# Optimization experiments

Measured on AMD Instinct MI355X. Metric: run time of the kernel, lower is better.

The kernel has to match this reference:

```python
import jax, jax.numpy as jnp
import numpy as np


def setup_inputs() -> dict:
    key = jax.random.key(0)
    k1, k2 = jax.random.split(key)
    B, C, H, W = 4, 256, 64, 64
    hw = 1024  # hs = ws = 32, rate = H/hs = 2
    ori_x = jax.random.normal(k1, (B, C, H, W), dtype=jnp.float32)
    scores = jax.random.uniform(k2, (B, hw, hw), dtype=jnp.float32)
    alpha = jnp.ones((1,), dtype=jnp.float32)
    return {"ori_x": ori_x, "scores": scores, "alpha": alpha}


def reference(ori_x, scores, alpha):
    # GroupConvAttention forward for H=W=64 (no bilinear resize branch taken,
    # matching the torch code's else-branch), rate even (no extra rep-pad).
    B, C, H, W = ori_x.shape
    hw = scores.shape[2]
    hs = int(np.sqrt(hw)); ws = hs
    rate = H // hs               # 2
    vk = 2 * rate                # vksize = 4
    pad = rate // 2              # vpadding = 1 (rate even)

    # extract_patches: ReplicationPad2d(pad) + unfold(kernel=vk, stride=rate)
    x_pad = jnp.pad(ori_x, ((0, 0), (0, 0), (pad, pad), (pad, pad)), mode="edge")
    # gather index grids: patch (m,n), intra-patch (u,v)
    ri = (jnp.arange(hs) * rate)[:, None] + jnp.arange(vk)[None, :]  # [hs, vk]
    ci = (jnp.arange(ws) * rate)[:, None] + jnp.arange(vk)[None, :]  # [ws, vk]
    R = ri[:, None, :, None]   # [hs,1,vk,1]
    Cc = ci[None, :, None, :]  # [1,ws,1,vk]
    value = x_pad[:, :, R, Cc]  # [B, C, hs, ws, vk, vk]

    # conv_transpose2d(scores_, value, stride=rate, padding=pad, groups=B)
    # == per query grid cell (Q,R): combined patch = sum_p scores[b,q,p]*value[b,p]
    s = scores.reshape(B, hs, ws, hs, ws)  # [b, Qy, Qx, my, mx]
    P = jnp.einsum("bQRmn,bcmnuv->bcQRuv", s, value)  # [B,C,hs,ws,vk,vk]

    # overlap-add patches at stride `rate` into padded canvas, then crop padding
    canvas = jnp.zeros((B, C, (hs - 1) * rate + vk, (ws - 1) * rate + vk), P.dtype)
    canvas = canvas.at[:, :, R, Cc].add(P)
    y = canvas[:, :, pad:pad + H, pad:pad + W] / 4.0

    return ori_x + y * alpha
```

## Files before the change

### kernel.cpp

```cpp
#include <hip/hip_runtime.h>
#include <hip/hip_bf16.h>
#include <hip/hip_fp16.h>

#define BB 4
#define CC 256
#define HH 64
#define WW 64
#define QRN 1024
#define KN  1024
#define KDIM 1152
#define TROWS 1089

typedef _Float16 f16x8 __attribute__((ext_vector_type(8)));
typedef float f32x4 __attribute__((ext_vector_type(4)));

#define TP_ELEMS ((size_t)BB * TROWS * KDIM)
#define BP_ELEMS ((size_t)16 * CC * KDIM)


__device__ __forceinline__
void process_qr(const float* __restrict__ sb, _Float16* __restrict__ T,
                int b, int qr, int t) {
    const int Qa = (qr * 993) >> 15;
    const int Ra = qr - 33 * Qa;
    const bool q0 = (Qa < 32), q1 = (Qa >= 1);
    const bool r0 = (Ra < 32), r1 = (Ra >= 1);
    const float* rb00 = sb + ((size_t)((Qa)     * 32 + (Ra)))     * KN;
    const float* rb01 = sb + ((size_t)((Qa)     * 32 + (Ra - 1))) * KN;
    const float* rb10 = sb + ((size_t)((Qa - 1) * 32 + (Ra)))     * KN;
    const float* rb11 = sb + ((size_t)((Qa - 1) * 32 + (Ra - 1))) * KN;
    _Float16* trow = T + ((size_t)b * TROWS + qr) * KDIM;

    float v[5];
    #pragma unroll
    for (int j = 0; j < 5; ++j) {
        const int k = j * 256 + t;
        v[j] = 0.f;
        if (k < KDIM) {
            const int mp = (k * 993) >> 15;
            const int np = k - 33 * mp;
            const bool m0 = (mp < 32), m1 = (mp >= 1) && (mp < 33);
            const bool n0 = (np < 32), n1 = (np >= 1);
            const int col = (mp << 5) + np;
            if (q0 & r0 & m0 & n0) v[j] += rb00[col];
            if (q0 & r1 & m0 & n1) v[j] += rb01[col - 1];
            if (q1 & r0 & m1 & n0) v[j] += rb10[col - 32];
            if (q1 & r1 & m1 & n1) v[j] += rb11[col - 33];
        }
    }
    #pragma unroll
    for (int j = 0; j < 5; ++j) {
        const int k = j * 256 + t;
        if (k < KDIM) trow[k] = (_Float16)v[j];
    }
}

#define T_BLOCKS 545
#define PER_B    705
#define TB_NWG   (BB * PER_B)

__global__ __launch_bounds__(256)
void build_TB(const float* __restrict__ s, const float* __restrict__ x,
              _Float16* __restrict__ T, _Float16* __restrict__ Bp) {
    const int orig = blockIdx.x;
    const int xcd = orig & 7, pos = orig >> 3;
    const int q = TB_NWG / 8, r = TB_NWG % 8;
    const int wgid =
        (xcd < r ? xcd * (q + 1) : r * (q + 1) + (xcd - r) * q) + pos;

    const int b = wgid / PER_B;
    const int rem = wgid - b * PER_B;
    const int t = threadIdx.x;

    if (rem < T_BLOCKS) {
        const float* sb = s + (size_t)b * QRN * KN;
        const int qr0 = rem * 2;
        process_qr(sb, T, b, qr0, t);
        if (qr0 + 1 < TROWS) process_qr(sb, T, b, qr0 + 1, t);
    } else {
        const int u = rem - T_BLOCKS;
        const int rest = u / 5;
        const int kc = u - rest * 5;
        const int cls = rest >> 3, cg = rest & 7;
        const int k = kc * 256 + t;
        if (k >= KDIM) return;
        const int ph = cls >> 1, pw = cls & 1;
        const int ua = 1 - ph, va = 1 - pw;
        const int bc = b * 4 + cls;

        const int mp = (k * 993) >> 15;
        const int np = k - 33 * mp;
        int rr = 2 * mp + ua - 1; rr = min(max(rr, 0), HH - 1);
        int cc2 = 2 * np + va - 1; cc2 = min(max(cc2, 0), WW - 1);
        const int off = rr * WW + cc2;

        const float* xb = x + ((size_t)b * CC + cg * 32) * HH * WW;
        _Float16* bpb = Bp + ((size_t)bc * CC + cg * 32) * KDIM + k;

        #pragma unroll 8
        for (int i = 0; i < 32; ++i) {
            bpb[(size_t)i * KDIM] = (_Float16)xb[(size_t)i * HH * WW + off];
        }
    }
}

__device__ __forceinline__ void gload16(const _Float16* g, _Float16* l) {
    __builtin_amdgcn_global_load_lds(
        (const __attribute__((address_space(1))) unsigned int*)g,
        (__attribute__((address_space(3))) unsigned int*)l, 16, 0, 0);
}

#define NSTEP  36
#define BUF_H  8192
__global__ __launch_bounds__(256, 1)
void gemm_f16(const _Float16* __restrict__ T,
              const _Float16* __restrict__ Bp,
              const float* __restrict__ orix,
              const float* __restrict__ alphap,
              float* __restrict__ out) {
    __shared__ __align__(16) _Float16 smem_h[8 * BUF_H];

    const int lin = blockIdx.x + 2 * (blockIdx.y + 8 * blockIdx.z);
    const int wid = (lin & 7) * 32 + (lin >> 3);
    const int bc  = wid >> 4;
    const int byy = (wid >> 1) & 7;
    const int bxx = wid & 1;

    const int b = bc >> 2, cls = bc & 3;
    const int ph = cls >> 1, pw = cls & 1;
    const int c0  = bxx * 128;
    const int px0 = byy * 128;

    const int t = threadIdx.x;
    const int wv = t >> 6, l = t & 63;
    const int lr = l & 15;
    const int lk = l >> 4;
    const int wr = wv >> 1, wc = wv & 1;

    const _Float16* Ag = Bp + ((size_t)bc * CC + c0) * KDIM;
    const _Float16* Tg = T + (size_t)b * TROWS * KDIM;

    const int st_row = t >> 2, st_slot = t & 3;
    const _Float16* srcA0 = Ag + (size_t)st_row * KDIM + st_slot * 8;
    const _Float16* srcA1 = Ag + (size_t)(st_row + 64) * KDIM + st_slot * 8;
    const int pxr0 = px0 + st_row, pxr1 = px0 + st_row + 64;
    const int trow0 = ((pxr0 >> 5) + ph) * 33 + (pxr0 & 31) + pw;
    const int trow1 = ((pxr1 >> 5) + ph) * 33 + (pxr1 & 31) + pw;
    const _Float16* srcB0 = Tg + (size_t)trow0 * KDIM + st_slot * 8;
    const _Float16* srcB1 = Tg + (size_t)trow1 * KDIM + st_slot * 8;
    _Float16* dst0 = smem_h + t * 8;
    _Float16* dst1 = smem_h + 2048 + t * 8;

    #define ISSUE(ts2)                                                     \
        do {                                                               \
            const int _bo = ((ts2) & 7) * BUF_H;                           \
            const int _k0 = (ts2) * 32;                                    \
            gload16(srcA0 + _k0, dst0 + _bo);                              \
            gload16(srcA1 + _k0, dst1 + _bo);                              \
            gload16(srcB0 + _k0, dst0 + _bo + 4096);                       \
            gload16(srcB1 + _k0, dst1 + _bo + 4096);                       \
        } while (0)

    f32x4 acc[4][4];
    #pragma unroll
    for (int i = 0; i < 4; ++i)
        #pragma unroll
        for (int j = 0; j < 4; ++j)
            acc[i][j] = (f32x4){0.f, 0.f, 0.f, 0.f};

    ISSUE(0); ISSUE(1); ISSUE(2); ISSUE(3); ISSUE(4); ISSUE(5); ISSUE(6);

    #pragma unroll
    for (int ts = 0; ts < NSTEP; ++ts) {
        asm volatile("s_waitcnt vmcnt(24)" ::: "memory");
        __builtin_amdgcn_s_barrier();
        const int nxt = (ts + 7 < NSTEP) ? ts + 7 : NSTEP - 1;
        ISSUE(nxt);

        const _Float16* ab = smem_h + (ts & 7) * BUF_H;
        const _Float16* bb = ab + 4096;
        f16x8 af[4], bf[4];
        #pragma unroll
        for (int mt = 0; mt < 4; ++mt)
            af[mt] = *(const f16x8*)(ab + (wr * 64 + mt * 16 + lr) * 32 + lk * 8);
        #pragma unroll
        for (int nt2 = 0; nt2 < 4; ++nt2)
            bf[nt2] = *(const f16x8*)(bb + (wc * 64 + nt2 * 16 + lr) * 32 + lk * 8);
        __builtin_amdgcn_s_setprio(1);
        #pragma unroll
        for (int mt = 0; mt < 4; ++mt)
            #pragma unroll
            for (int nt2 = 0; nt2 < 4; ++nt2)
                acc[mt][nt2] = __builtin_amdgcn_mfma_f32_16x16x32_f16(
                    af[mt], bf[nt2], acc[mt][nt2], 0, 0, 0);
        __builtin_amdgcn_s_setprio(0);
    }
    #undef ISSUE
    asm volatile("s_waitcnt vmcnt(0)" ::: "memory");

    const float scale = 0.25f * alphap[0];
    #pragma unroll
    for (int mt = 0; mt < 4; ++mt) {
        #pragma unroll
        for (int nt2 = 0; nt2 < 4; ++nt2) {
            #pragma unroll
            for (int r2 = 0; r2 < 4; ++r2) {
                int c  = c0 + wr * 64 + mt * 16 + lk * 4 + r2;
                int px = px0 + wc * 64 + nt2 * 16 + lr;
                int hh = px >> 5, ww2 = px & 31;
                int h = 2 * hh + ph, wp = 2 * ww2 + pw;
                size_t idx = (((size_t)b * CC + c) * HH + h) * WW + wp;
                out[idx] = orix[idx] + scale * acc[mt][nt2][r2];
            }
        }
    }
}

#define TILE_M 64
#define TILE_N 64
#define TILE_K 16

__global__ void copy_kernel(const float* __restrict__ src,
                            float* __restrict__ dst, int n4) {
    int i = blockIdx.x * blockDim.x + threadIdx.x;
    if (i < n4)
        reinterpret_cast<float4*>(dst)[i] =
            reinterpret_cast<const float4*>(src)[i];
}

__global__ void transpose_kernel(const float* __restrict__ x,
                                 float* __restrict__ xT) {
    __shared__ float tile[32][33];
    int bh = blockIdx.z;
    int b = bh >> 6, h = bh & 63;
    int c0 = blockIdx.y * 32, w0 = blockIdx.x * 32;
    int tw = threadIdx.x & 31;
    int tc = threadIdx.x >> 5;
    #pragma unroll
    for (int i = 0; i < 4; ++i) {
        int c = tc + i * 8;
        tile[c][tw] = x[(((size_t)b * CC + c0 + c) * HH + h) * WW + w0 + tw];
    }
    __syncthreads();
    int tcw = threadIdx.x & 31;
    int twr = threadIdx.x >> 5;
    #pragma unroll
    for (int i = 0; i < 4; ++i) {
        int w = twr + i * 8;
        xT[(((size_t)b * HH + h) * WW + w0 + w) * CC + c0 + tcw] = tile[tcw][w];
    }
}

__global__ __launch_bounds__(256)
void pgemm_scatter(const float* __restrict__ scores,
                   const float* __restrict__ xT,
                   const float* __restrict__ x,
                   const float* __restrict__ alpha,
                   float* __restrict__ out,
                   int use_xt) {
    __shared__ float As[TILE_K][TILE_M];
    __shared__ float Bs[TILE_K][TILE_N];

    const int b      = blockIdx.z;
    const int tile_n = blockIdx.x;
    const int m0     = blockIdx.y * TILE_M;
    const int uv     = tile_n >> 2;
    const int u      = uv >> 2, v = uv & 3;
    const int c0     = (tile_n & 3) * 64;

    const int t  = threadIdx.x;
    const int tx = t & 15;
    const int ty = t >> 4;

    float acc[4][4] = {};
    const float* sb = scores + (size_t)b * QRN * KN;

    for (int k0 = 0; k0 < KN; k0 += TILE_K) {
        {
            int mr = t >> 2;
            int kc = (t & 3) * 4;
            float4 av = *reinterpret_cast<const float4*>(
                sb + (size_t)(m0 + mr) * KN + k0 + kc);
            As[kc + 0][mr] = av.x;
            As[kc + 1][mr] = av.y;
            As[kc + 2][mr] = av.z;
            As[kc + 3][mr] = av.w;
        }
        {
            int kr = t >> 4;
            int kg = k0 + kr;
            int m  = kg >> 5, n = kg & 31;
            int rr = 2 * m + u - 1; rr = min(max(rr, 0), HH - 1);
            int cc = 2 * n + v - 1; cc = min(max(cc, 0), WW - 1);
            int ccol = (t & 15) * 4;
            if (use_xt) {
                float4 bv = *reinterpret_cast<const float4*>(
                    xT + ((((size_t)b * HH + rr) * WW + cc) * CC) + c0 + ccol);
                Bs[kr][ccol + 0] = bv.x;
                Bs[kr][ccol + 1] = bv.y;
                Bs[kr][ccol + 2] = bv.z;
                Bs[kr][ccol + 3] = bv.w;
            } else {
                #pragma unroll
                for (int j = 0; j < 4; ++j) {
                    int c = c0 + ccol + j;
                    Bs[kr][ccol + j] =
                        x[(((size_t)b * CC + c) * HH + rr) * WW + cc];
                }
            }
        }
        __syncthreads();

        #pragma unroll
        for (int k = 0; k < TILE_K; ++k) {
            float a4[4], b4[4];
            *reinterpret_cast<float4*>(a4) =
                *reinterpret_cast<const float4*>(&As[k][ty * 4]);
            *reinterpret_cast<float4*>(b4) =
                *reinterpret_cast<const float4*>(&Bs[k][tx * 4]);
            #pragma unroll
            for (int i = 0; i < 4; ++i)
                #pragma unroll
                for (int j = 0; j < 4; ++j)
                    acc[i][j] += a4[i] * b4[j];
        }
        __syncthreads();
    }

    const float scale = alpha[0] * 0.25f;
    #pragma unroll
    for (int i = 0; i < 4; ++i) {
        int qr = m0 + ty * 4 + i;
        int Q = qr >> 5, R = qr & 31;
        int h = 2 * Q + u - 1;
        int w = 2 * R + v - 1;
        if (h < 0 || h >= HH || w < 0 || w >= WW) continue;
        #pragma unroll
        for (int j = 0; j < 4; ++j) {
            int c = c0 + tx * 4 + j;
            atomicAdd(&out[(((size_t)b * CC + c) * HH + h) * WW + w],
                      acc[i][j] * scale);
        }
    }
}

extern "C" void kernel_launch(void* const* d_in, const int* in_sizes, int n_in,
                              void* d_out, int out_size, void* d_ws,
                              size_t ws_size, hipStream_t stream) {
    const float* ori_x  = (const float*)d_in[0];
    const float* scores = (const float*)d_in[1];
    const float* alpha  = (const float*)d_in[2];
    float* out = (float*)d_out;

    const size_t need_fast = (TP_ELEMS + BP_ELEMS) * sizeof(_Float16);

    if (ws_size >= need_fast) {
        _Float16* T  = (_Float16*)d_ws;
        _Float16* Bp = T + TP_ELEMS;

        build_TB<<<dim3(TB_NWG), 256, 0, stream>>>(scores, ori_x, T, Bp);
        gemm_f16<<<dim3(2, 8, 16), 256, 0, stream>>>(T, Bp, ori_x, alpha, out);
    } else {
        float* xT = (float*)d_ws;
        const size_t xt_bytes = (size_t)BB * HH * WW * CC * sizeof(float);
        const int use_xt = (ws_size >= xt_bytes) ? 1 : 0;

        copy_kernel<<<(BB * CC * HH * WW / 4 + 255) / 256, 256, 0, stream>>>(
            ori_x, out, BB * CC * HH * WW / 4);
        if (use_xt)
            transpose_kernel<<<dim3(WW / 32, CC / 32, BB * HH), 256, 0,
                               stream>>>(ori_x, xT);
        pgemm_scatter<<<dim3(16, 16, BB), 256, 0, stream>>>(
            scores, xT, ori_x, alpha, out, use_xt);
    }
}
```

Measured before the change: 45.93 us.

## Fuse build and GEMM kernels into one cooperative launch with grid sync

Merges the T/Bp build kernel and the f16 MFMA GEMM into a single persistent cooperative kernel of 256 workgroups. Each workgroup first loops over build tasks with a stride, then a grid-wide sync separates this from the GEMM phase. The aim is to remove one kernel launch and the inter-kernel gap. In exchange, the build phase now runs on only 256 workgroups, each limited to one per CU with a large LDS allocation, instead of 2820 smaller ones. That may lower memory-level parallelism during the build, and the grid sync adds its own cost.

Result: slower. 171.5 us (+273.4%).

```diff
diff --git a/kernel.cpp b/kernel.cpp
--- a/kernel.cpp
+++ b/kernel.cpp
@@ -1,6 +1,9 @@
 #include <hip/hip_runtime.h>
+#include <hip/hip_cooperative_groups.h>
 #include <hip/hip_bf16.h>
 #include <hip/hip_fp16.h>
+
+namespace cg = cooperative_groups;
 
 #define BB 4
 #define CC 256
@@ -55,72 +58,71 @@
     }
 }
 
-#define T_BLOCKS 545
-#define PER_B    705
-#define TB_NWG   (BB * PER_B)
-
-__global__ __launch_bounds__(256)
-void build_TB(const float* __restrict__ s, const float* __restrict__ x,
-              _Float16* __restrict__ T, _Float16* __restrict__ Bp) {
-    const int orig = blockIdx.x;
-    const int xcd = orig & 7, pos = orig >> 3;
-    const int q = TB_NWG / 8, r = TB_NWG % 8;
-    const int wgid =
-        (xcd < r ? xcd * (q + 1) : r * (q + 1) + (xcd - r) * q) + pos;
-
-    const int b = wgid / PER_B;
-    const int rem = wgid - b * PER_B;
-    const int t = threadIdx.x;
-
-    if (rem < T_BLOCKS) {
-        const float* sb = s + (size_t)b * QRN * KN;
-        const int qr0 = rem * 2;
-        process_qr(sb, T, b, qr0, t);
-        if (qr0 + 1 < TROWS) process_qr(sb, T, b, qr0 + 1, t);
-    } else {
-        const int u = rem - T_BLOCKS;
-        const int rest = u / 5;
-        const int kc = u - rest * 5;
-        const int cls = rest >> 3, cg = rest & 7;
-        const int k = kc * 256 + t;
-        if (k >= KDIM) return;
-        const int ph = cls >> 1, pw = cls & 1;
-        const int ua = 1 - ph, va = 1 - pw;
-        const int bc = b * 4 + cls;
-
-        const int mp = (k * 993) >> 15;
-        const int np = k - 33 * mp;
-        int rr = 2 * mp + ua - 1; rr = min(max(rr, 0), HH - 1);
-        int cc2 = 2 * np + va - 1; cc2 = min(max(cc2, 0), WW - 1);
-        const int off = rr * WW + cc2;
-
-        const float* xb = x + ((size_t)b * CC + cg * 32) * HH * WW;
-        _Float16* bpb = Bp + ((size_t)bc * CC + cg * 32) * KDIM + k;
-
-        #pragma unroll 8
-        for (int i = 0; i < 32; ++i) {
-            bpb[(size_t)i * KDIM] = (_Float16)xb[(size_t)i * HH * WW + off];
-        }
-    }
-}
-
 __device__ __forceinline__ void gload16(const _Float16* g, _Float16* l) {
     __builtin_amdgcn_global_load_lds(
         (const __attribute__((address_space(1))) unsigned int*)g,
         (__attribute__((address_space(3))) unsigned int*)l, 16, 0, 0);
 }
 
+#define T_BLOCKS 545
+#define PER_B    705
 #define NSTEP  36
 #define BUF_H  8192
+
 __global__ __launch_bounds__(256, 1)
-void gemm_f16(const _Float16* __restrict__ T,
-              const _Float16* __restrict__ Bp,
-              const float* __restrict__ orix,
-              const float* __restrict__ alphap,
-              float* __restrict__ out) {
+void fused_tb_gemm(const float* __restrict__ s,
+                   const float* __restrict__ x,
+                   const float* __restrict__ orix,
+                   const float* __restrict__ alphap,
+                   _Float16* __restrict__ T,
+                   _Float16* __restrict__ Bp,
+                   float* __restrict__ out) {
     __shared__ __align__(16) _Float16 smem_h[8 * BUF_H];
 
-    const int lin = blockIdx.x + 2 * (blockIdx.y + 8 * blockIdx.z);
+    const int lin = blockIdx.x;
+    const int t = threadIdx.x;
+
+    {
+        const int xcd = lin & 7;
+        const int bb = xcd >> 1;
+        const int start = (xcd & 1) * 32 + (lin >> 3);
+        const float* sb = s + (size_t)bb * QRN * KN;
+
+        for (int j = start; j < PER_B; j += 64) {
+            if (j < T_BLOCKS) {
+                const int qr0 = j * 2;
+                process_qr(sb, T, bb, qr0, t);
+                if (qr0 + 1 < TROWS) process_qr(sb, T, bb, qr0 + 1, t);
+            } else {
+                const int u = j - T_BLOCKS;
+                const int rest = u / 5;
+                const int kc = u - rest * 5;
+                const int cls = rest >> 3, cg2 = rest & 7;
+                const int k = kc * 256 + t;
+                if (k < KDIM) {
+                    const int ph = cls >> 1, pw = cls & 1;
+                    const int ua = 1 - ph, va = 1 - pw;
+                    const int bc = bb * 4 + cls;
+                    const int mp = (k * 993) >> 15;
+                    const int np = k - 33 * mp;
+                    int rr = 2 * mp + ua - 1; rr = min(max(rr, 0), HH - 1);
+                    int cc2 = 2 * np + va - 1; cc2 = min(max(cc2, 0), WW - 1);
+                    const int off = rr * WW + cc2;
+                    const float* xb = x + ((size_t)bb * CC + cg2 * 32) * HH * WW;
+                    _Float16* bpb = Bp + ((size_t)bc * CC + cg2 * 32) * KDIM + k;
+                    #pragma unroll 8
+                    for (int i = 0; i < 32; ++i) {
+                        bpb[(size_t)i * KDIM] =
+                            (_Float16)xb[(size_t)i * HH * WW + off];
+                    }
+                }
+            }
+        }
+    }
+
+    __threadfence();
+    cg::this_grid().sync();
+
     const int wid = (lin & 7) * 32 + (lin >> 3);
     const int bc  = wid >> 4;
     const int byy = (wid >> 1) & 7;
@@ -131,7 +133,6 @@
     const int c0  = bxx * 128;
     const int px0 = byy * 128;
 
-    const int t = threadIdx.x;
     const int wv = t >> 6, l = t & 63;
     const int lr = l & 15;
     const int lk = l >> 4;
@@ -178,14 +179,14 @@
         ISSUE(nxt);
 
         const _Float16* ab = smem_h + (ts & 7) * BUF_H;
-        const _Float16* bb = ab + 4096;
+        const _Float16* bb2 = ab + 4096;
         f16x8 af[4], bf[4];
         #pragma unroll
         for (int mt = 0; mt < 4; ++mt)
             af[mt] = *(const f16x8*)(ab + (wr * 64 + mt * 16 + lr) * 32 + lk * 8);
         #pragma unroll
         for (int nt2 = 0; nt2 < 4; ++nt2)
-            bf[nt2] = *(const f16x8*)(bb + (wc * 64 + nt2 * 16 + lr) * 32 + lk * 8);
+            bf[nt2] = *(const f16x8*)(bb2 + (wc * 64 + nt2 * 16 + lr) * 32 + lk * 8);
         __builtin_amdgcn_s_setprio(1);
         #pragma unroll
         for (int mt = 0; mt < 4; ++mt)
@@ -358,8 +359,17 @@
         _Float16* T  = (_Float16*)d_ws;
         _Float16* Bp = T + TP_ELEMS;
 
-        build_TB<<<dim3(TB_NWG), 256, 0, stream>>>(scores, ori_x, T, Bp);
-        gemm_f16<<<dim3(2, 8, 16), 256, 0, stream>>>(T, Bp, ori_x, alpha, out);
+        const float* s_  = scores;
+        const float* x_  = ori_x;
+        const float* ox_ = ori_x;
+        const float* al_ = alpha;
+        _Float16* T_  = T;
+        _Float16* Bp_ = Bp;
+        float* out_ = out;
+        void* args[] = {(void*)&s_, (void*)&x_, (void*)&ox_, (void*)&al_,
+                        (void*)&T_, (void*)&Bp_, (void*)&out_};
+        hipLaunchCooperativeKernel((const void*)fused_tb_gemm,
+                                   dim3(256), dim3(256), args, 0, stream);
     } else {
         float* xT = (float*)d_ws;
         const size_t xt_bytes = (size_t)BB * HH * WW * CC * sizeof(float);
```
